# Kernel optimization log

Hardware: AMD Instinct MI355X
Metric: run time of the kernel (lower is better)

## Reference

```python
import jax, jax.numpy as jnp
import numpy as np

EPS = 1e-8  # matches F.cosine_similarity default eps
SIM_TARGET = 1  # int(self.sim_matrix), a scalar constant


def setup_inputs() -> dict:
    key = jax.random.key(0)
    k1, k2 = jax.random.split(key)
    input1 = jax.random.normal(k1, (4096, 1024), dtype=jnp.float32)  # [U, P]
    input2 = jax.random.normal(k2, (4096, 1024), dtype=jnp.float32)  # [V, P]
    return {"input1": input1, "input2": input2}


def reference(input1, input2):
    # Row-normalize with eps clamp (same as F.cosine_similarity per pair)
    n1 = input1 / jnp.maximum(jnp.linalg.norm(input1, axis=1, keepdims=True), EPS)
    n2 = input2 / jnp.maximum(jnp.linalg.norm(input2, axis=1, keepdims=True), EPS)
    cos = jnp.einsum('up,vp->uv', n1, n2)  # [U, V] pairwise cosine similarity
    return jnp.sum((SIM_TARGET - cos) ** 2)
```

## Files before the change

### kernel.cpp

```cpp
#include <hip/hip_runtime.h>
#include <hip/hip_bf16.h>
#include <stdint.h>

#define U_ROWS 4096
#define P_DIM  1024
#define TILE   128
#define BK     64

typedef float f32x4 __attribute__((ext_vector_type(4)));
typedef long  lx2   __attribute__((ext_vector_type(2)));

__global__ __launch_bounds__(256) void norm_fp8_kernel(
    const float* __restrict__ in1, const float* __restrict__ in2,
    uint8_t* __restrict__ out, float* __restrict__ loss_out) {
    const int w = threadIdx.x >> 6, lane = threadIdx.x & 63;
    const int row = blockIdx.x * 4 + w;
    const float* src = (row < U_ROWS) ? (in1 + (size_t)row * P_DIM)
                                      : (in2 + (size_t)(row - U_ROWS) * P_DIM);
    float4 v[4];
    float ss = 0.0f;
    #pragma unroll
    for (int j = 0; j < 4; ++j) {
        v[j] = ((const float4*)src)[j * 64 + lane];
        ss += v[j].x * v[j].x + v[j].y * v[j].y + v[j].z * v[j].z + v[j].w * v[j].w;
    }
    #pragma unroll
    for (int off = 32; off > 0; off >>= 1) ss += __shfl_xor(ss, off, 64);
    const float inv = 16.0f / fmaxf(sqrtf(ss), 1e-8f);

    uint8_t* orow = out + (size_t)row * P_DIM;
    #pragma unroll
    for (int j = 0; j < 4; ++j) {
        int c = j * 256 + lane * 4;
        int pos = (c & 4) + (((c >> 3) & 3) * 16) + (((c >> 5) & 1) * 8);
        int newc = (c & ~63) | pos;
        int d = __builtin_amdgcn_cvt_pk_fp8_f32(v[j].x * inv, v[j].y * inv, 0, false);
        d = __builtin_amdgcn_cvt_pk_fp8_f32(v[j].z * inv, v[j].w * inv, d, true);
        *(int*)(orow + newc) = d;
    }
    if (blockIdx.x == 0 && threadIdx.x == 0) *loss_out = 0.0f;
}

__global__ __launch_bounds__(256) void cosloss_gemm_fp8(
    const uint8_t* __restrict__ n1, const uint8_t* __restrict__ n2,
    float* __restrict__ loss_out) {
    __shared__ uint8_t As[TILE * BK];
    __shared__ uint8_t Bs[TILE * BK];
    __shared__ float red[4];

    const int tid  = threadIdx.x;
    const int w    = tid >> 6;
    const int lane = tid & 63;

    const int id  = blockIdx.y * gridDim.x + blockIdx.x;
    const int xcd = id & 7;
    const int j   = id >> 3;
    const int cb  = xcd * 4 + (j & 3);
    const int rb  = j >> 2;

    const uint8_t* gA = n1 + (size_t)rb * TILE * P_DIM;
    const uint8_t* gB = n2 + (size_t)cb * TILE * P_DIM;

    const uint8_t* gbase = (w < 2) ? gA : gB;
    uint8_t* sbase = (w < 2) ? As : Bs;
    const int i0   = (w & 1) * 4;
    const int srow = lane >> 2;
    const int scol = (lane & 3) * 16;

    f32x4 acc[4][4];
    #pragma unroll
    for (int mi = 0; mi < 4; ++mi)
        #pragma unroll
        for (int ni = 0; ni < 4; ++ni)
            acc[mi][ni] = (f32x4){0.f, 0.f, 0.f, 0.f};

    const int wr = (w >> 1) * 64;
    const int wc = (w & 1) * 64;
    const int fr = lane & 15;
    const int q  = lane >> 4;

    for (int kt = 0; kt < P_DIM / BK; ++kt) {
        #pragma unroll
        for (int ii = 0; ii < 4; ++ii) {
            const int is = i0 + ii;
            const uint8_t* g =
                gbase + (size_t)(is * 16 + srow) * P_DIM + kt * BK + scol;
            __builtin_amdgcn_global_load_lds(
                (const __attribute__((address_space(1))) void*)g,
                (__attribute__((address_space(3))) void*)(sbase + is * 1024),
                16, 0, 0);
        }
        __syncthreads();

        lx2 af[4], bfr[4];
        #pragma unroll
        for (int i = 0; i < 4; ++i) {
            af[i]  = *(const lx2*)(As + (wr + i * 16 + fr) * BK + q * 16);
            bfr[i] = *(const lx2*)(Bs + (wc + i * 16 + fr) * BK + q * 16);
        }
        #pragma unroll
        for (int mi = 0; mi < 4; ++mi)
            #pragma unroll
            for (int ni = 0; ni < 4; ++ni) {
                acc[mi][ni] = __builtin_amdgcn_mfma_f32_16x16x32_fp8_fp8(
                    af[mi].x, bfr[ni].x, acc[mi][ni], 0, 0, 0);
                acc[mi][ni] = __builtin_amdgcn_mfma_f32_16x16x32_fp8_fp8(
                    af[mi].y, bfr[ni].y, acc[mi][ni], 0, 0, 0);
            }
        __syncthreads();
    }

    float local = 0.0f;
    #pragma unroll
    for (int mi = 0; mi < 4; ++mi)
        #pragma unroll
        for (int ni = 0; ni < 4; ++ni)
            #pragma unroll
            for (int r = 0; r < 4; ++r) {
                const float d = 1.0f - acc[mi][ni][r] * (1.0f / 256.0f);
                local += d * d;
            }
    #pragma unroll
    for (int off = 32; off > 0; off >>= 1) local += __shfl_down(local, off, 64);
    if (lane == 0) red[w] = local;
    __syncthreads();
    if (tid == 0) atomicAdd(loss_out, red[0] + red[1] + red[2] + red[3]);
}

extern "C" void kernel_launch(void* const* d_in, const int* in_sizes, int n_in,
                              void* d_out, int out_size, void* d_ws, size_t ws_size,
                              hipStream_t stream) {
    const float* in1 = (const float*)d_in[0];
    const float* in2 = (const float*)d_in[1];
    float* out = (float*)d_out;
    uint8_t* nrm = (uint8_t*)d_ws;

    norm_fp8_kernel<<<(U_ROWS * 2) / 4, 256, 0, stream>>>(in1, in2, nrm, out);

    dim3 grid(U_ROWS / TILE, U_ROWS / TILE);
    cosloss_gemm_fp8<<<grid, 256, 0, stream>>>(
        nrm, nrm + (size_t)U_ROWS * P_DIM, out);
}
```

Before: 104.2 us.

## Load FP8 GEMM fragments directly from global memory with register prefetch

Drops the LDS staging and both per-iteration barriers in the FP8 MFMA GEMM. Each wave now loads its A/B fragments straight from global memory into registers and prefetches the next K slice while the current MFMAs run. The goal is to remove sync and LDS round-trip overhead, but each operand is now fetched by two waves instead of being shared through LDS, which doubles global/L2 traffic. It also raises register pressure. The grid is flattened to 1D, which keeps the same block-id swizzle.

```diff
diff --git a/kernel.cpp b/kernel.cpp
--- a/kernel.cpp
+++ b/kernel.cpp
@@ -44,28 +44,25 @@
 __global__ __launch_bounds__(256) void cosloss_gemm_fp8(
     const uint8_t* __restrict__ n1, const uint8_t* __restrict__ n2,
     float* __restrict__ loss_out) {
-    __shared__ uint8_t As[TILE * BK];
-    __shared__ uint8_t Bs[TILE * BK];
     __shared__ float red[4];
 
     const int tid  = threadIdx.x;
     const int w    = tid >> 6;
     const int lane = tid & 63;
 
-    const int id  = blockIdx.y * gridDim.x + blockIdx.x;
+    const int id  = blockIdx.x;
     const int xcd = id & 7;
     const int j   = id >> 3;
     const int cb  = xcd * 4 + (j & 3);
     const int rb  = j >> 2;
 
-    const uint8_t* gA = n1 + (size_t)rb * TILE * P_DIM;
-    const uint8_t* gB = n2 + (size_t)cb * TILE * P_DIM;
+    const int wr = (w >> 1) * 64;
+    const int wc = (w & 1) * 64;
+    const int fr = lane & 15;
+    const int q  = lane >> 4;
 
-    const uint8_t* gbase = (w < 2) ? gA : gB;
-    uint8_t* sbase = (w < 2) ? As : Bs;
-    const int i0   = (w & 1) * 4;
-    const int srow = lane >> 2;
-    const int scol = (lane & 3) * 16;
+    const uint8_t* pa = n1 + (size_t)(rb * TILE + wr + fr) * P_DIM + q * 16;
+    const uint8_t* pb = n2 + (size_t)(cb * TILE + wc + fr) * P_DIM + q * 16;
 
     f32x4 acc[4][4];
     #pragma unroll
@@ -74,40 +71,33 @@
         for (int ni = 0; ni < 4; ++ni)
             acc[mi][ni] = (f32x4){0.f, 0.f, 0.f, 0.f};
 
-    const int wr = (w >> 1) * 64;
-    const int wc = (w & 1) * 64;
-    const int fr = lane & 15;
-    const int q  = lane >> 4;
+    lx2 ca[4], cbf[4], na[4], nb[4];
+    #pragma unroll
+    for (int i = 0; i < 4; ++i) {
+        ca[i]  = *(const lx2*)(pa + (size_t)i * 16 * P_DIM);
+        cbf[i] = *(const lx2*)(pb + (size_t)i * 16 * P_DIM);
+    }
 
+    #pragma unroll
     for (int kt = 0; kt < P_DIM / BK; ++kt) {
-        #pragma unroll
-        for (int ii = 0; ii < 4; ++ii) {
-            const int is = i0 + ii;
-            const uint8_t* g =
-                gbase + (size_t)(is * 16 + srow) * P_DIM + kt * BK + scol;
-            __builtin_amdgcn_global_load_lds(
-                (const __attribute__((address_space(1))) void*)g,
-                (__attribute__((address_space(3))) void*)(sbase + is * 1024),
-                16, 0, 0);
-        }
-        __syncthreads();
-
-        lx2 af[4], bfr[4];
-        #pragma unroll
-        for (int i = 0; i < 4; ++i) {
-            af[i]  = *(const lx2*)(As + (wr + i * 16 + fr) * BK + q * 16);
-            bfr[i] = *(const lx2*)(Bs + (wc + i * 16 + fr) * BK + q * 16);
+        if (kt + 1 < P_DIM / BK) {
+            #pragma unroll
+            for (int i = 0; i < 4; ++i) {
+                na[i] = *(const lx2*)(pa + (size_t)i * 16 * P_DIM + (kt + 1) * BK);
+                nb[i] = *(const lx2*)(pb + (size_t)i * 16 * P_DIM + (kt + 1) * BK);
+            }
         }
         #pragma unroll
         for (int mi = 0; mi < 4; ++mi)
             #pragma unroll
             for (int ni = 0; ni < 4; ++ni) {
                 acc[mi][ni] = __builtin_amdgcn_mfma_f32_16x16x32_fp8_fp8(
-                    af[mi].x, bfr[ni].x, acc[mi][ni], 0, 0, 0);
+                    ca[mi].x, cbf[ni].x, acc[mi][ni], 0, 0, 0);
                 acc[mi][ni] = __builtin_amdgcn_mfma_f32_16x16x32_fp8_fp8(
-                    af[mi].y, bfr[ni].y, acc[mi][ni], 0, 0, 0);
+                    ca[mi].y, cbf[ni].y, acc[mi][ni], 0, 0, 0);
             }
-        __syncthreads();
+        #pragma unroll
+        for (int i = 0; i < 4; ++i) { ca[i] = na[i]; cbf[i] = nb[i]; }
     }
 
     float local = 0.0f;
@@ -117,14 +107,15 @@
         for (int ni = 0; ni < 4; ++ni)
             #pragma unroll
             for (int r = 0; r < 4; ++r) {
-                const float d = 1.0f - acc[mi][ni][r] * (1.0f / 256.0f);
-                local += d * d;
+                const float dd = 1.0f - acc[mi][ni][r] * (1.0f / 256.0f);
+                local += dd * dd;
             }
     #pragma unroll
     for (int off = 32; off > 0; off >>= 1) local += __shfl_down(local, off, 64);
     if (lane == 0) red[w] = local;
     __syncthreads();
-    if (tid == 0) atomicAdd(loss_out, red[0] + red[1] + red[2] + red[3]);
+    if (tid == 0)
+        atomicAdd(loss_out, red[0] + red[1] + red[2] + red[3]);
 }
 
 extern "C" void kernel_launch(void* const* d_in, const int* in_sizes, int n_in,
@@ -137,7 +128,6 @@
 
     norm_fp8_kernel<<<(U_ROWS * 2) / 4, 256, 0, stream>>>(in1, in2, nrm, out);
 
-    dim3 grid(U_ROWS / TILE, U_ROWS / TILE);
-    cosloss_gemm_fp8<<<grid, 256, 0, stream>>>(
+    cosloss_gemm_fp8<<<(U_ROWS / TILE) * (U_ROWS / TILE), 256, 0, stream>>>(
         nrm, nrm + (size_t)U_ROWS * P_DIM, out);
 }
```

Result: slower. 155.2 us (+49.0%).
